# Kernel optimization log

Measured on AMD Instinct MI355X. Metric: run time of the kernel, lower is better.

The kernel has to match this reference:

```python
import jax, jax.numpy as jnp
import numpy as np

B, S, DM, H, SD = 8, 2048, 512, 8, 64
INNER = H * SD
HID = 4 * DM
EPS = 1e-5


def setup_inputs() -> dict:
    key = jax.random.key(0)
    ks = jax.random.split(key, 12)
    p = lambda k, sh: jax.random.normal(k, sh, dtype=jnp.float32) * 0.02
    return {
        "x": jax.random.normal(ks[0], (B, S, DM), dtype=jnp.float32),
        "norm_g": jnp.ones((DM,), jnp.float32),
        "norm_b": jnp.zeros((DM,), jnp.float32),
        "ffn_norm_g": jnp.ones((DM,), jnp.float32),
        "ffn_norm_b": jnp.zeros((DM,), jnp.float32),
        "Wa": p(ks[1], (INNER, DM)),
        "Wb": p(ks[2], (INNER, DM)),
        "Wql": p(ks[3], (INNER, DM)),
        "Wqr": p(ks[4], (INNER, DM)),
        "Wsd": p(ks[5], (H, DM)),
        "bsd": jnp.zeros((H,), jnp.float32),
        "Wpd": p(ks[6], (H, DM)),
        "bpd": jnp.zeros((H,), jnp.float32),
        "Wout": p(ks[7], (DM, INNER)),
        "W1": p(ks[8], (HID, DM)),
        "b1": jnp.zeros((HID,), jnp.float32),
        "W2": p(ks[9], (DM, HID)),
        "b2": jnp.zeros((DM,), jnp.float32),
    }


def _ln(x, g, b):
    m = x.mean(-1, keepdims=True)
    v = ((x - m) ** 2).mean(-1, keepdims=True)
    return (x - m) / jnp.sqrt(v + EPS) * g + b


def reference(x, norm_g, norm_b, ffn_norm_g, ffn_norm_b, Wa, Wb, Wql, Wqr,
              Wsd, bsd, Wpd, bpd, Wout, W1, b1, W2, b2):
    n = _ln(x, norm_g, norm_b)  # [B,S,DM]
    # project, reshape to heads, move time axis first for scan: [S,B,H,SD]
    tm = lambda t: t.reshape(B, S, H, SD).transpose(1, 0, 2, 3)
    a_all = tm(jnp.tanh(n @ Wa.T))
    b_all = tm(jnp.tanh(n @ Wb.T))
    ql_all = tm(jnp.tanh(n @ Wql.T))
    qr_all = tm(jnp.tanh(n @ Wqr.T))
    sd_all = jax.nn.sigmoid(n @ Wsd.T + bsd).transpose(1, 0, 2)[..., None]        # [S,B,H,1]
    pd_all = jax.nn.sigmoid(n @ Wpd.T + bpd).transpose(1, 0, 2)[..., None, None]  # [S,B,H,1,1]

    def step(carry, inp):
        state, pair = carry  # state [B,H,SD], pair [B,H,SD,SD]
        at, bt, qlt, sdt, pdt = inp
        prev = state
        state = sdt * state + (1.0 - sdt) * at
        pair = pdt * pair + (1.0 - pdt) * jnp.einsum('bhd,bhe->bhde', prev, bt)
        lc = jnp.einsum('bhde,bhd->bhe', pair, qlt)  # left context [B,H,SD]
        return (state, pair), lc

    init = (jnp.zeros((B, H, SD), x.dtype), jnp.zeros((B, H, SD, SD), x.dtype))
    _, lc = jax.lax.scan(step, init, (a_all, b_all, ql_all, sd_all, pd_all))  # [S,B,H,SD]

    mixed = ((lc * qr_all).transpose(1, 0, 2, 3).reshape(B, S, INNER)) @ Wout.T  # [B,S,DM]
    r = x + mixed  # dropout is identity in eval
    h = jax.nn.gelu(_ln(r, ffn_norm_g, ffn_norm_b) @ W1.T + b1, approximate=False)
    return r + h @ W2.T + b2
```

## Files before the change

### kernel.cpp

```cpp
#include <hip/hip_runtime.h>
#include <cstdint>
#include <cstddef>

#define B_    8
#define S_    2048
#define DM_   512
#define H_    8
#define SD_   64
#define HID_  2048
#define ROWS  (B_*S_)
#define BH    (B_*H_)
#define NCHUNK 32
#define CLEN   64
#define EPS_  1e-5f

typedef __bf16 bf16x8 __attribute__((ext_vector_type(8)));
typedef float  floatx4 __attribute__((ext_vector_type(4)));

static __device__ __forceinline__ float bf2f(unsigned short h){
  union { unsigned int u; float f; } v; v.u = ((unsigned int)h) << 16; return v.f;
}
static __device__ __forceinline__ unsigned short f2bf(float f){
  union { float f; unsigned int u; } v; v.f = f;
  unsigned int r = v.u + 0x7fffu + ((v.u >> 16) & 1u);
  return (unsigned short)(r >> 16);
}
static __device__ __forceinline__ float fast_tanh(float x){
  float ax = fabsf(x);
  float e  = __expf(2.f*ax);
  float t  = 1.f - 2.f/(e+1.f);
  return copysignf(t, x);
}
static __device__ __forceinline__ float sigmoidf_(float z){
  return 1.f/(1.f + expf(-z));
}
static __device__ __forceinline__ float gelu_exact(float x){
  return 0.5f*x*(1.f + erff(x*0.70710678118654752440f));
}
static __device__ __forceinline__ void gld_lds16(const unsigned short* g, unsigned short* lds){
  __builtin_amdgcn_global_load_lds(
      (const __attribute__((address_space(1))) void*)g,
      (__attribute__((address_space(3))) void*)lds,
      16, 0, 0);
}
static __device__ __forceinline__ int swz(int row, int col){
  return row*64 + (((col>>3) ^ (row&7))<<3) + (col&7);
}

__global__ __launch_bounds__(256) void cvt_weights(
    const float* __restrict__ wa, const float* __restrict__ wb,
    const float* __restrict__ wql, const float* __restrict__ wqr,
    const float* __restrict__ wout, const float* __restrict__ w1,
    const float* __restrict__ w2,
    unsigned short* __restrict__ wcat, unsigned short* __restrict__ woutb,
    unsigned short* __restrict__ w1b, unsigned short* __restrict__ w2b){
  int i = blockIdx.x*256 + threadIdx.x;
  const float* s; unsigned short* d; int base;
  if      (i <  65536){ s=wa;   d=wcat;          base=i; }
  else if (i < 131072){ s=wb;   d=wcat+262144;   base=i-65536; }
  else if (i < 196608){ s=wql;  d=wcat+524288;   base=i-131072; }
  else if (i < 262144){ s=wqr;  d=wcat+786432;   base=i-196608; }
  else if (i < 327680){ s=wout; d=woutb;         base=i-262144; }
  else if (i < 589824){ s=w1;   d=w1b;           base=i-327680; }
  else                { s=w2;   d=w2b;           base=i-589824; }
  float4 v = ((const float4*)s)[base];
  ushort4 o; o.x=f2bf(v.x); o.y=f2bf(v.y); o.z=f2bf(v.z); o.w=f2bf(v.w);
  ((ushort4*)d)[base] = o;
}

__global__ __launch_bounds__(64) void ln_gates(
    const float* __restrict__ x, const float* __restrict__ gam, const float* __restrict__ bet,
    const float* __restrict__ Wsd, const float* __restrict__ bsd,
    const float* __restrict__ Wpd, const float* __restrict__ bpd,
    unsigned short* __restrict__ nbf, float* __restrict__ sdo, float* __restrict__ pdo){
  const int row = blockIdx.x, l = threadIdx.x;
  const float* xr = x + (size_t)row*DM_;
  float4 v0 = ((const float4*)xr)[l*2];
  float4 v1 = ((const float4*)xr)[l*2+1];
  float v[8] = {v0.x,v0.y,v0.z,v0.w,v1.x,v1.y,v1.z,v1.w};
  float s = 0.f;
  #pragma unroll
  for (int i=0;i<8;++i) s += v[i];
  #pragma unroll
  for (int m=1;m<64;m<<=1) s += __shfl_xor(s, m);
  const float mean = s * (1.f/512.f);
  float q = 0.f;
  #pragma unroll
  for (int i=0;i<8;++i){ float d = v[i]-mean; q += d*d; }
  #pragma unroll
  for (int m=1;m<64;m<<=1) q += __shfl_xor(q, m);
  const float rstd = rsqrtf(q*(1.f/512.f) + EPS_);
  float4 g0 = ((const float4*)gam)[l*2], g1 = ((const float4*)gam)[l*2+1];
  float4 b0 = ((const float4*)bet)[l*2], b1 = ((const float4*)bet)[l*2+1];
  float gg[8] = {g0.x,g0.y,g0.z,g0.w,g1.x,g1.y,g1.z,g1.w};
  float bb[8] = {b0.x,b0.y,b0.z,b0.w,b1.x,b1.y,b1.z,b1.w};
  float n[8];
  #pragma unroll
  for (int i=0;i<8;++i) n[i] = (v[i]-mean)*rstd*gg[i] + bb[i];
  ushort4 o0, o1;
  o0.x=f2bf(n[0]); o0.y=f2bf(n[1]); o0.z=f2bf(n[2]); o0.w=f2bf(n[3]);
  o1.x=f2bf(n[4]); o1.y=f2bf(n[5]); o1.z=f2bf(n[6]); o1.w=f2bf(n[7]);
  ((ushort4*)(nbf + (size_t)row*DM_))[l*2]   = o0;
  ((ushort4*)(nbf + (size_t)row*DM_))[l*2+1] = o1;
  float acc[16];
  #pragma unroll
  for (int hh=0; hh<8; ++hh){
    const float4* ws = (const float4*)(Wsd + hh*DM_) + l*2;
    const float4* wp = (const float4*)(Wpd + hh*DM_) + l*2;
    float4 a0=ws[0], a1=ws[1], p0=wp[0], p1=wp[1];
    acc[hh]   = n[0]*a0.x+n[1]*a0.y+n[2]*a0.z+n[3]*a0.w+n[4]*a1.x+n[5]*a1.y+n[6]*a1.z+n[7]*a1.w;
    acc[8+hh] = n[0]*p0.x+n[1]*p0.y+n[2]*p0.z+n[3]*p0.w+n[4]*p1.x+n[5]*p1.y+n[6]*p1.z+n[7]*p1.w;
  }
  #pragma unroll
  for (int k=0;k<16;++k){
    float a = acc[k];
    #pragma unroll
    for (int m=1;m<64;m<<=1) a += __shfl_xor(a, m);
    acc[k] = a;
  }
  if (l==0){
    #pragma unroll
    for (int hh=0; hh<8; ++hh){
      sdo[row*8+hh] = sigmoidf_(acc[hh]   + bsd[hh]);
      pdo[row*8+hh] = sigmoidf_(acc[8+hh] + bpd[hh]);
    }
  }
}

__global__ __launch_bounds__(64) void ln_plain(
    const float* __restrict__ x, const float* __restrict__ gam, const float* __restrict__ bet,
    unsigned short* __restrict__ ob){
  const int row = blockIdx.x, l = threadIdx.x;
  const float* xr = x + (size_t)row*DM_;
  float4 v0 = ((const float4*)xr)[l*2];
  float4 v1 = ((const float4*)xr)[l*2+1];
  float v[8] = {v0.x,v0.y,v0.z,v0.w,v1.x,v1.y,v1.z,v1.w};
  float s = 0.f;
  #pragma unroll
  for (int i=0;i<8;++i) s += v[i];
  #pragma unroll
  for (int m=1;m<64;m<<=1) s += __shfl_xor(s, m);
  const float mean = s * (1.f/512.f);
  float q = 0.f;
  #pragma unroll
  for (int i=0;i<8;++i){ float d = v[i]-mean; q += d*d; }
  #pragma unroll
  for (int m=1;m<64;m<<=1) q += __shfl_xor(q, m);
  const float rstd = rsqrtf(q*(1.f/512.f) + EPS_);
  float4 g0 = ((const float4*)gam)[l*2], g1 = ((const float4*)gam)[l*2+1];
  float4 b0 = ((const float4*)bet)[l*2], b1 = ((const float4*)bet)[l*2+1];
  float gg[8] = {g0.x,g0.y,g0.z,g0.w,g1.x,g1.y,g1.z,g1.w};
  float bb[8] = {b0.x,b0.y,b0.z,b0.w,b1.x,b1.y,b1.z,b1.w};
  ushort4 o0, o1;
  float n0=(v[0]-mean)*rstd*gg[0]+bb[0], n1=(v[1]-mean)*rstd*gg[1]+bb[1];
  float n2=(v[2]-mean)*rstd*gg[2]+bb[2], n3=(v[3]-mean)*rstd*gg[3]+bb[3];
  float n4=(v[4]-mean)*rstd*gg[4]+bb[4], n5=(v[5]-mean)*rstd*gg[5]+bb[5];
  float n6=(v[6]-mean)*rstd*gg[6]+bb[6], n7=(v[7]-mean)*rstd*gg[7]+bb[7];
  o0.x=f2bf(n0); o0.y=f2bf(n1); o0.z=f2bf(n2); o0.w=f2bf(n3);
  o1.x=f2bf(n4); o1.y=f2bf(n5); o1.z=f2bf(n6); o1.w=f2bf(n7);
  ((ushort4*)(ob + (size_t)row*DM_))[l*2]   = o0;
  ((ushort4*)(ob + (size_t)row*DM_))[l*2+1] = o1;
}

template<int MODE>
__global__ __launch_bounds__(256) void gemm128(
    const unsigned short* __restrict__ A, const unsigned short* __restrict__ W,
    const float* __restrict__ bias, const float* __restrict__ resid,
    float* __restrict__ outf, unsigned short* __restrict__ outb,
    int N, int K){
  __shared__ __align__(16) unsigned short As[128*64];
  __shared__ __align__(16) unsigned short Ws[128*64];
  const int tid  = threadIdx.x;
  const int w    = tid >> 6;
  const int lane = tid & 63;
  const int mblk = blockIdx.x, nblk = blockIdx.y;
  const int mrow = (w >> 1) * 64;
  const int ncol = (w & 1) * 64;
  const int fr = lane & 15, fq = lane >> 4;

  int srow[4], scol[4];
  #pragma unroll
  for (int q=0;q<4;++q){
    const int p = q*256 + w*64 + lane;
    srow[q] = p >> 3;
    scol[q] = ((p & 7) ^ (srow[q] & 7)) * 8;
  }

  floatx4 acc[4][4];
  #pragma unroll
  for (int i=0;i<4;++i)
    #pragma unroll
    for (int j=0;j<4;++j)
      acc[i][j] = (floatx4){0.f,0.f,0.f,0.f};

  for (int k0=0; k0<K; k0+=64){
    #pragma unroll
    for (int q=0;q<4;++q){
      gld_lds16(A + (size_t)(mblk*128 + srow[q])*K + k0 + scol[q], As + (q*256 + w*64)*8);
      gld_lds16(W + (size_t)(nblk*128 + srow[q])*K + k0 + scol[q], Ws + (q*256 + w*64)*8);
    }
    __syncthreads();
    #pragma unroll
    for (int kh=0;kh<2;++kh){
      bf16x8 af[4], bf[4];
      #pragma unroll
      for (int i=0;i<4;++i) af[i] = *(const bf16x8*)&As[swz(mrow + i*16 + fr, kh*32 + fq*8)];
      #pragma unroll
      for (int j=0;j<4;++j) bf[j] = *(const bf16x8*)&Ws[swz(ncol + j*16 + fr, kh*32 + fq*8)];
      #pragma unroll
      for (int i=0;i<4;++i)
        #pragma unroll
        for (int j=0;j<4;++j)
          acc[i][j] = __builtin_amdgcn_mfma_f32_16x16x32_bf16(af[i], bf[j], acc[i][j], 0, 0, 0);
    }
    __syncthreads();
  }

  #pragma unroll
  for (int i=0;i<4;++i){
    const int grow_base = mblk*128 + mrow + i*16 + fq*4;
    #pragma unroll
    for (int j=0;j<4;++j){
      const int gcol = nblk*128 + ncol + j*16 + fr;
      float bias_v = 0.f;
      if (MODE==2 || MODE==3) bias_v = bias[gcol];
      #pragma unroll
      for (int r=0;r<4;++r){
        const size_t o = (size_t)(grow_base + r)*N + gcol;
        float v = acc[i][j][r];
        if      (MODE==0) outb[o] = f2bf(fast_tanh(v));
        else if (MODE==1) outf[o] = resid[o] + v;
        else if (MODE==2) outb[o] = f2bf(gelu_exact(v + bias_v));
        else              outf[o] = resid[o] + v + bias_v;
      }
    }
  }
}

__global__ __launch_bounds__(64) void state_local(
    const unsigned short* __restrict__ proj, const float* __restrict__ sdo,
    unsigned short* __restrict__ slocb, float* __restrict__ Sarr,
    float* __restrict__ sEnd){
  const int c = blockIdx.x, bh = blockIdx.y, b = bh>>3, h = bh&7, d = threadIdx.x;
  float s = 0.f, S = 1.f;
  const int t0 = c*CLEN;
  #pragma unroll 4
  for (int j=0;j<CLEN;++j){
    const int t = t0 + j;
    float a  = bf2f(proj[((size_t)(b*S_+t))*2048 + h*64 + d]);
    float sv = sdo[(b*S_+t)*8 + h];
    s = sv*s + (1.f-sv)*a;
    S *= sv;
    slocb[((size_t)bh*S_ + t)*64 + d] = f2bf(s);
    if (d==0) Sarr[bh*S_ + t] = S;
  }
  sEnd[((size_t)c*BH + bh)*64 + d] = s;
}

__global__ __launch_bounds__(64) void state_combine(
    const float* __restrict__ sEnd, const float* __restrict__ Sarr,
    float* __restrict__ sinit){
  const int bh = blockIdx.x, d = threadIdx.x;
  float acc = 0.f;
  for (int c=0;c<NCHUNK;++c){
    sinit[((size_t)c*BH + bh)*64 + d] = acc;
    const int te = c*CLEN + CLEN - 1;
    acc = Sarr[bh*S_ + te]*acc + sEnd[((size_t)c*BH + bh)*64 + d];
  }
}

__global__ __launch_bounds__(256) void prev_mat(
    const unsigned short* __restrict__ slocb, const float* __restrict__ Sarr,
    const float* __restrict__ sinit, unsigned short* __restrict__ prevb){
  const size_t idx = (size_t)blockIdx.x*256 + threadIdx.x;
  const int d  = (int)(idx & 63);
  const size_t bt = idx >> 6;
  const int t  = (int)(bt & (S_-1));
  const int bh = (int)(bt >> 11);
  const int c = t >> 6, j = t & 63;
  float init = sinit[((size_t)c*BH + bh)*64 + d];
  float p;
  if (j==0) p = init;
  else {
    const size_t pt = (size_t)bh*S_ + (t-1);
    p = Sarr[pt]*init + bf2f(slocb[pt*64 + d]);
  }
  prevb[idx] = f2bf(p);
}

__global__ __launch_bounds__(64) void pair_localm(
    const unsigned short* __restrict__ proj, const float* __restrict__ pdo,
    const unsigned short* __restrict__ prevb, float* __restrict__ pairbuf,
    float* __restrict__ Dprod){
  __shared__ __align__(16) unsigned short Bt[4096];
  __shared__ __align__(16) unsigned short Pt[4096];
  const int c=blockIdx.x, bh=blockIdx.y, b=bh>>3, h=bh&7, l=threadIdx.x;
  const int t = c*CLEN + l;
  float pd = pdo[(b*S_+t)*8 + h];
  float D = pd;
  #pragma unroll
  for (int m=1;m<64;m<<=1){ float o = __shfl_up(D, m); if (l>=m) D *= o; }
  const float Dend = __shfl(D, 63);
  const float cu = (Dend / D) * (1.f - pd);
  if (l==63) Dprod[c*BH+bh] = Dend;
  {
    const unsigned short* brow = proj  + ((size_t)(b*S_+t))*2048 + 512 + h*64;
    const unsigned short* prow = prevb + ((size_t)bh*S_ + t)*64;
    #pragma unroll
    for (int e8=0;e8<8;++e8){
      ushort4 u0 = *(const ushort4*)(brow + e8*8);
      ushort4 u1 = *(const ushort4*)(brow + e8*8 + 4);
      unsigned short vs[8] = {u0.x,u0.y,u0.z,u0.w,u1.x,u1.y,u1.z,u1.w};
      ushort4 p0 = *(const ushort4*)(prow + e8*8);
      ushort4 p1 = *(const ushort4*)(prow + e8*8 + 4);
      unsigned short ps[8] = {p0.x,p0.y,p0.z,p0.w,p1.x,p1.y,p1.z,p1.w};
      #pragma unroll
      for (int q=0;q<8;++q){
        const int r = e8*8+q;
        Bt[swz(r, l)] = f2bf(cu * bf2f(vs[q]));
        Pt[swz(r, l)] = ps[q];
      }
    }
  }
  __syncthreads();
  const int fr = l & 15, fq = l >> 4;
  floatx4 acc[4][4];
  #pragma unroll
  for (int i=0;i<4;++i)
    #pragma unroll
    for (int j=0;j<4;++j) acc[i][j] = (floatx4){0.f,0.f,0.f,0.f};
  #pragma unroll
  for (int kh=0;kh<2;++kh){
    bf16x8 af[4], bfr[4];
    #pragma unroll
    for (int i=0;i<4;++i) af[i]  = *(const bf16x8*)&Bt[swz(i*16+fr, kh*32+fq*8)];
    #pragma unroll
    for (int j=0;j<4;++j) bfr[j] = *(const bf16x8*)&Pt[swz(j*16+fr, kh*32+fq*8)];
    #pragma unroll
    for (int i=0;i<4;++i)
      #pragma unroll
      for (int j=0;j<4;++j)
        acc[i][j] = __builtin_amdgcn_mfma_f32_16x16x32_bf16(af[i], bfr[j], acc[i][j], 0, 0, 0);
  }
  float* outp = pairbuf + ((size_t)c*BH + bh)*4096;
  #pragma unroll
  for (int i=0;i<4;++i)
    #pragma unroll
    for (int j=0;j<4;++j)
      #pragma unroll
      for (int r=0;r<4;++r)
        outp[(i*16+fq*4+r)*64 + j*16+fr] = acc[i][j][r];
}

__global__ __launch_bounds__(256) void pair_combine(
    float* __restrict__ pairbuf, const float* __restrict__ Dprod){
  const int idx = blockIdx.x*256 + threadIdx.x;
  const int de = idx & 4095, bh = idx >> 12;
  float acc = 0.f;
  for (int c=0;c<NCHUNK;++c){
    const size_t o = ((size_t)c*BH + bh)*4096 + de;
    float loc = pairbuf[o];
    pairbuf[o] = acc;
    acc = Dprod[c*BH + bh]*acc + loc;
  }
}

__global__ __launch_bounds__(64) void pair_finalm(
    const unsigned short* __restrict__ proj, const float* __restrict__ pdo,
    const unsigned short* __restrict__ prevb, const float* __restrict__ pinit,
    unsigned short* __restrict__ lcqr){
  __shared__ __align__(16) unsigned short Bt[4096];
  __shared__ __align__(16) unsigned short Tb[4096];
  __shared__ __align__(16) float Dtl[64];
  __shared__ __align__(16) float cudl[64];
  const int c=blockIdx.x, bh=blockIdx.y, b=bh>>3, h=bh&7, l=threadIdx.x;
  const int t0 = c*CLEN;
  const int trow = t0 + l;
  float pd = pdo[(b*S_+trow)*8 + h];
  float D = pd;
  #pragma unroll
  for (int m=1;m<64;m<<=1){ float o = __shfl_up(D, m); if (l>=m) D *= o; }
  Dtl[l]  = D;
  cudl[l] = (1.f - pd) / D;
  {
    const unsigned short* brow = proj + ((size_t)(b*S_+trow))*2048 + 512 + h*64;
    #pragma unroll
    for (int e8=0;e8<8;++e8){
      ushort4 u0 = *(const ushort4*)(brow + e8*8);
      ushort4 u1 = *(const ushort4*)(brow + e8*8 + 4);
      unsigned short vs[8] = {u0.x,u0.y,u0.z,u0.w,u1.x,u1.y,u1.z,u1.w};
      #pragma unroll
      for (int q=0;q<8;++q) Bt[swz(e8*8+q, l)] = vs[q];
    }
  }
  __syncthreads();
  const int fr = l & 15, fq = l >> 4;
  bf16x8 qf[4][2], pf[4][2];
  #pragma unroll
  for (int i=0;i<4;++i)
    #pragma unroll
    for (int kh=0;kh<2;++kh){
      qf[i][kh] = *(const bf16x8*)(proj  + ((size_t)(b*S_ + t0 + i*16 + fr))*2048 + 1024 + h*64 + kh*32 + fq*8);
      pf[i][kh] = *(const bf16x8*)(prevb + ((size_t)(bh*S_ + t0 + i*16 + fr))*64  + kh*32 + fq*8);
    }
  floatx4 sacc[4][4];
  #pragma unroll
  for (int i=0;i<4;++i)
    #pragma unroll
    for (int j=0;j<4;++j) sacc[i][j] = (floatx4){0.f,0.f,0.f,0.f};
  #pragma unroll
  for (int kh=0;kh<2;++kh)
    #pragma unroll
    for (int i=0;i<4;++i)
      #pragma unroll
      for (int j=0;j<4;++j)
        sacc[i][j] = __builtin_amdgcn_mfma_f32_16x16x32_bf16(qf[i][kh], pf[j][kh], sacc[i][j], 0, 0, 0);
  float mycud[4];
  #pragma unroll
  for (int j=0;j<4;++j) mycud[j] = cudl[j*16+fr];
  #pragma unroll
  for (int i=0;i<4;++i){
    floatx4 dtv = *(const floatx4*)&Dtl[i*16+fq*4];
    #pragma unroll
    for (int j=0;j<4;++j){
      const int uu = j*16+fr;
      #pragma unroll
      for (int r=0;r<4;++r){
        const int tt = i*16+fq*4+r;
        float v = (uu<=tt) ? (sacc[i][j][r]*dtv[r])*mycud[j] : 0.f;
        Tb[swz(tt, uu)] = f2bf(v);
      }
    }
  }
  __syncthreads();
  floatx4 acc[4][4];
  #pragma unroll
  for (int i=0;i<4;++i)
    #pragma unroll
    for (int j=0;j<4;++j) acc[i][j] = (floatx4){0.f,0.f,0.f,0.f};
  #pragma unroll
  for (int kh=0;kh<2;++kh){
    bf16x8 af[4], bfr[4];
    #pragma unroll
    for (int i=0;i<4;++i) af[i]  = *(const bf16x8*)&Tb[swz(i*16+fr, kh*32+fq*8)];
    #pragma unroll
    for (int j=0;j<4;++j) bfr[j] = *(const bf16x8*)&Bt[swz(j*16+fr, kh*32+fq*8)];
    #pragma unroll
    for (int i=0;i<4;++i)
      #pragma unroll
      for (int j=0;j<4;++j)
        acc[i][j] = __builtin_amdgcn_mfma_f32_16x16x32_bf16(af[i], bfr[j], acc[i][j], 0, 0, 0);
  }
  {
    const float* ibase = pinit + ((size_t)c*BH + bh)*4096;
    #pragma unroll
    for (int kh=0;kh<2;++kh){
      bf16x8 qs[4], inf[4];
      #pragma unroll
      for (int i=0;i<4;++i){
        const float sc = Dtl[i*16+fr];
        #pragma unroll
        for (int e=0;e<8;++e) qs[i][e] = (__bf16)(sc * (float)qf[i][kh][e]);
      }
      #pragma unroll
      for (int j=0;j<4;++j){
        const float* ip = ibase + (j*16+fr)*64 + kh*32 + fq*8;
        float4 f0 = *(const float4*)ip;
        float4 f1 = *(const float4*)(ip+4);
        inf[j][0]=(__bf16)f0.x; inf[j][1]=(__bf16)f0.y; inf[j][2]=(__bf16)f0.z; inf[j][3]=(__bf16)f0.w;
        inf[j][4]=(__bf16)f1.x; inf[j][5]=(__bf16)f1.y; inf[j][6]=(__bf16)f1.z; inf[j][7]=(__bf16)f1.w;
      }
      #pragma unroll
      for (int i=0;i<4;++i)
        #pragma unroll
        for (int j=0;j<4;++j)
          acc[i][j] = __builtin_amdgcn_mfma_f32_16x16x32_bf16(qs[i], inf[j], acc[i][j], 0, 0, 0);
    }
  }
  __syncthreads();
  #pragma unroll
  for (int i=0;i<4;++i)
    #pragma unroll
    for (int j=0;j<4;++j)
      #pragma unroll
      for (int r=0;r<4;++r)
        Tb[swz(i*16+fq*4+r, j*16+fr)] = f2bf(acc[i][j][r]);
  __syncthreads();
  {
    const unsigned short* qrow = proj + ((size_t)(b*S_+trow))*2048 + 1536 + h*64;
    unsigned short* orow = lcqr + ((size_t)(b*S_+trow))*512 + h*64;
    #pragma unroll
    for (int e8=0;e8<8;++e8){
      bf16x8 lcv = *(const bf16x8*)&Tb[swz(l, e8*8)];
      ushort4 q0 = *(const ushort4*)(qrow + e8*8);
      ushort4 q1 = *(const ushort4*)(qrow + e8*8 + 4);
      unsigned short qv[8] = {q0.x,q0.y,q0.z,q0.w,q1.x,q1.y,q1.z,q1.w};
      ushort4 o0, o1;
      o0.x = f2bf((float)lcv[0]*bf2f(qv[0]));
      o0.y = f2bf((float)lcv[1]*bf2f(qv[1]));
      o0.z = f2bf((float)lcv[2]*bf2f(qv[2]));
      o0.w = f2bf((float)lcv[3]*bf2f(qv[3]));
      o1.x = f2bf((float)lcv[4]*bf2f(qv[4]));
      o1.y = f2bf((float)lcv[5]*bf2f(qv[5]));
      o1.z = f2bf((float)lcv[6]*bf2f(qv[6]));
      o1.w = f2bf((float)lcv[7]*bf2f(qv[7]));
      *(ushort4*)(orow + e8*8)     = o0;
      *(ushort4*)(orow + e8*8 + 4) = o1;
    }
  }
}

extern "C" void kernel_launch(void* const* d_in, const int* in_sizes, int n_in,
                              void* d_out, int out_size, void* d_ws, size_t ws_size,
                              hipStream_t stream){
  (void)in_sizes; (void)n_in; (void)out_size; (void)ws_size;
  const float* x    = (const float*)d_in[0];
  const float* ng   = (const float*)d_in[1];
  const float* nb   = (const float*)d_in[2];
  const float* fng  = (const float*)d_in[3];
  const float* fnb  = (const float*)d_in[4];
  const float* Wa   = (const float*)d_in[5];
  const float* Wb   = (const float*)d_in[6];
  const float* Wql  = (const float*)d_in[7];
  const float* Wqr  = (const float*)d_in[8];
  const float* Wsd  = (const float*)d_in[9];
  const float* bsd  = (const float*)d_in[10];
  const float* Wpd  = (const float*)d_in[11];
  const float* bpd  = (const float*)d_in[12];
  const float* Wout = (const float*)d_in[13];
  const float* W1   = (const float*)d_in[14];
  const float* b1   = (const float*)d_in[15];
  const float* W2   = (const float*)d_in[16];
  const float* b2   = (const float*)d_in[17];
  float* out = (float*)d_out;
  char* ws = (char*)d_ws;

  size_t off = 0;
  auto alloc = [&](size_t bytes)->char*{ char* p = ws + off; off += (bytes + 255) & ~(size_t)255; return p; };
  char* RA = alloc((size_t)ROWS*DM_*2);
  char* RB = alloc((size_t)ROWS*2048*2);
  char* RD = alloc((size_t)BH*S_*64*4);
  char* RE = alloc((size_t)BH*S_*64*4);
  float* sdo   = (float*)alloc((size_t)ROWS*8*4);
  float* pdo   = (float*)alloc((size_t)ROWS*8*4);
  float* Sarr  = (float*)alloc((size_t)BH*S_*4);
  float* sinit = (float*)alloc((size_t)NCHUNK*BH*64*4);
  float* sEnd  = (float*)alloc((size_t)NCHUNK*BH*64*4);
  float* dprod = (float*)alloc((size_t)NCHUNK*BH*4);
  unsigned short* wcat  = (unsigned short*)alloc((size_t)2048*512*2);
  unsigned short* woutb = (unsigned short*)alloc((size_t)512*512*2);
  unsigned short* w1b   = (unsigned short*)alloc((size_t)2048*512*2);
  unsigned short* w2b   = (unsigned short*)alloc((size_t)512*2048*2);

  unsigned short* nbf   = (unsigned short*)RA;
  unsigned short* lcqr  = (unsigned short*)RA;
  unsigned short* nr    = (unsigned short*)RA;
  unsigned short* proj  = (unsigned short*)RB;
  unsigned short* hbuf  = (unsigned short*)RB;
  unsigned short* slocb = (unsigned short*)RD;
  float* pairb = (float*)RD;
  unsigned short* prevb = (unsigned short*)RE;
  float* rbuf  = (float*)RE;

  cvt_weights<<<dim3(3328), dim3(256), 0, stream>>>(Wa,Wb,Wql,Wqr,Wout,W1,W2, wcat,woutb,w1b,w2b);
  ln_gates<<<dim3(ROWS), dim3(64), 0, stream>>>(x, ng, nb, Wsd, bsd, Wpd, bpd, nbf, sdo, pdo);
  gemm128<0><<<dim3(128,16), dim3(256), 0, stream>>>(nbf, wcat, nullptr, nullptr, nullptr, proj, 2048, 512);
  state_local<<<dim3(NCHUNK,BH), dim3(64), 0, stream>>>(proj, sdo, slocb, Sarr, sEnd);
  state_combine<<<dim3(BH), dim3(64), 0, stream>>>(sEnd, Sarr, sinit);
  prev_mat<<<dim3(32768), dim3(256), 0, stream>>>(slocb, Sarr, sinit, prevb);
  pair_localm<<<dim3(NCHUNK,BH), dim3(64), 0, stream>>>(proj, pdo, prevb, pairb, dprod);
  pair_combine<<<dim3(1024), dim3(256), 0, stream>>>(pairb, dprod);
  pair_finalm<<<dim3(NCHUNK,BH), dim3(64), 0, stream>>>(proj, pdo, prevb, pairb, lcqr);
  gemm128<1><<<dim3(128,4), dim3(256), 0, stream>>>(lcqr, woutb, nullptr, x, rbuf, nullptr, 512, 512);
  ln_plain<<<dim3(ROWS), dim3(64), 0, stream>>>(rbuf, fng, fnb, nr);
  gemm128<2><<<dim3(128,16), dim3(256), 0, stream>>>(nr, w1b, b1, nullptr, nullptr, hbuf, 2048, 512);
  gemm128<3><<<dim3(128,4), dim3(256), 0, stream>>>(hbuf, w2b, b2, rbuf, out, nullptr, 512, 2048);
}
```

Baseline: 446.2 us.

## Use 256x256 tiles for wide GEMMs and store residual in bf16

Adds a gemm256 kernel with 512-thread blocks and 256x256 output tiles, used for the two N=2048 projections (QKV-like tanh projection and FFN up with GELU). Each block loads twice as many rows and columns per K step, so operand reuse per LDS load goes up and global traffic goes down. Separately, the residual buffer r is now stored as bf16 instead of fp32, which halves its write and read traffic in the Wout GEMM, the LayerNorm and the final GEMM. The cost is more registers per thread and fewer blocks (512 per GEMM), plus bf16 rounding of the residual stream added to the output.

```diff
diff --git a/kernel.cpp b/kernel.cpp
--- a/kernel.cpp
+++ b/kernel.cpp
@@ -128,13 +128,14 @@
 }
 
 __global__ __launch_bounds__(64) void ln_plain(
-    const float* __restrict__ x, const float* __restrict__ gam, const float* __restrict__ bet,
+    const unsigned short* __restrict__ xb, const float* __restrict__ gam, const float* __restrict__ bet,
     unsigned short* __restrict__ ob){
   const int row = blockIdx.x, l = threadIdx.x;
-  const float* xr = x + (size_t)row*DM_;
-  float4 v0 = ((const float4*)xr)[l*2];
-  float4 v1 = ((const float4*)xr)[l*2+1];
-  float v[8] = {v0.x,v0.y,v0.z,v0.w,v1.x,v1.y,v1.z,v1.w};
+  const unsigned short* xr = xb + (size_t)row*DM_ + l*8;
+  ushort4 u0 = *(const ushort4*)xr;
+  ushort4 u1 = *(const ushort4*)(xr+4);
+  float v[8] = {bf2f(u0.x),bf2f(u0.y),bf2f(u0.z),bf2f(u0.w),
+                bf2f(u1.x),bf2f(u1.y),bf2f(u1.z),bf2f(u1.w)};
   float s = 0.f;
   #pragma unroll
   for (int i=0;i<8;++i) s += v[i];
@@ -152,20 +153,91 @@
   float gg[8] = {g0.x,g0.y,g0.z,g0.w,g1.x,g1.y,g1.z,g1.w};
   float bb[8] = {b0.x,b0.y,b0.z,b0.w,b1.x,b1.y,b1.z,b1.w};
   ushort4 o0, o1;
-  float n0=(v[0]-mean)*rstd*gg[0]+bb[0], n1=(v[1]-mean)*rstd*gg[1]+bb[1];
-  float n2=(v[2]-mean)*rstd*gg[2]+bb[2], n3=(v[3]-mean)*rstd*gg[3]+bb[3];
-  float n4=(v[4]-mean)*rstd*gg[4]+bb[4], n5=(v[5]-mean)*rstd*gg[5]+bb[5];
-  float n6=(v[6]-mean)*rstd*gg[6]+bb[6], n7=(v[7]-mean)*rstd*gg[7]+bb[7];
-  o0.x=f2bf(n0); o0.y=f2bf(n1); o0.z=f2bf(n2); o0.w=f2bf(n3);
-  o1.x=f2bf(n4); o1.y=f2bf(n5); o1.z=f2bf(n6); o1.w=f2bf(n7);
+  o0.x=f2bf((v[0]-mean)*rstd*gg[0]+bb[0]); o0.y=f2bf((v[1]-mean)*rstd*gg[1]+bb[1]);
+  o0.z=f2bf((v[2]-mean)*rstd*gg[2]+bb[2]); o0.w=f2bf((v[3]-mean)*rstd*gg[3]+bb[3]);
+  o1.x=f2bf((v[4]-mean)*rstd*gg[4]+bb[4]); o1.y=f2bf((v[5]-mean)*rstd*gg[5]+bb[5]);
+  o1.z=f2bf((v[6]-mean)*rstd*gg[6]+bb[6]); o1.w=f2bf((v[7]-mean)*rstd*gg[7]+bb[7]);
   ((ushort4*)(ob + (size_t)row*DM_))[l*2]   = o0;
   ((ushort4*)(ob + (size_t)row*DM_))[l*2+1] = o1;
+}
+
+template<int MODE>
+__global__ __launch_bounds__(512, 2) void gemm256(
+    const unsigned short* __restrict__ A, const unsigned short* __restrict__ W,
+    const float* __restrict__ bias, unsigned short* __restrict__ outb,
+    int N, int K){
+  __shared__ __align__(16) unsigned short As[256*64];
+  __shared__ __align__(16) unsigned short Ws[256*64];
+  const int tid  = threadIdx.x;
+  const int w    = tid >> 6;
+  const int lane = tid & 63;
+  const int mblk = blockIdx.x, nblk = blockIdx.y;
+  const int mrow = (w >> 1) * 64;
+  const int ncol = (w & 1) * 128;
+  const int fr = lane & 15, fq = lane >> 4;
+
+  int srow[4], scol[4];
+  #pragma unroll
+  for (int q=0;q<4;++q){
+    const int p = q*512 + tid;
+    srow[q] = p >> 3;
+    scol[q] = ((p & 7) ^ (srow[q] & 7)) * 8;
+  }
+
+  floatx4 acc[4][8];
+  #pragma unroll
+  for (int i=0;i<4;++i)
+    #pragma unroll
+    for (int j=0;j<8;++j)
+      acc[i][j] = (floatx4){0.f,0.f,0.f,0.f};
+
+  for (int k0=0; k0<K; k0+=64){
+    #pragma unroll
+    for (int q=0;q<4;++q){
+      gld_lds16(A + (size_t)(mblk*256 + srow[q])*K + k0 + scol[q], As + (q*512 + tid)*8);
+      gld_lds16(W + (size_t)(nblk*256 + srow[q])*K + k0 + scol[q], Ws + (q*512 + tid)*8);
+    }
+    __syncthreads();
+    #pragma unroll
+    for (int kh=0;kh<2;++kh){
+      bf16x8 af[4], bf[8];
+      #pragma unroll
+      for (int i=0;i<4;++i) af[i] = *(const bf16x8*)&As[swz(mrow + i*16 + fr, kh*32 + fq*8)];
+      #pragma unroll
+      for (int j=0;j<8;++j) bf[j] = *(const bf16x8*)&Ws[swz(ncol + j*16 + fr, kh*32 + fq*8)];
+      #pragma unroll
+      for (int i=0;i<4;++i)
+        #pragma unroll
+        for (int j=0;j<8;++j)
+          acc[i][j] = __builtin_amdgcn_mfma_f32_16x16x32_bf16(af[i], bf[j], acc[i][j], 0, 0, 0);
+    }
+    __syncthreads();
+  }
+
+  #pragma unroll
+  for (int i=0;i<4;++i){
+    const int grow_base = mblk*256 + mrow + i*16 + fq*4;
+    #pragma unroll
+    for (int j=0;j<8;++j){
+      const int gcol = nblk*256 + ncol + j*16 + fr;
+      float bias_v = 0.f;
+      if (MODE==2) bias_v = bias[gcol];
+      #pragma unroll
+      for (int r=0;r<4;++r){
+        const size_t o = (size_t)(grow_base + r)*N + gcol;
+        float v = acc[i][j][r];
+        if (MODE==0) outb[o] = f2bf(fast_tanh(v));
+        else         outb[o] = f2bf(gelu_exact(v + bias_v));
+      }
+    }
+  }
 }
 
 template<int MODE>
 __global__ __launch_bounds__(256) void gemm128(
     const unsigned short* __restrict__ A, const unsigned short* __restrict__ W,
-    const float* __restrict__ bias, const float* __restrict__ resid,
+    const float* __restrict__ bias, const float* __restrict__ residf,
+    const unsigned short* __restrict__ residb,
     float* __restrict__ outf, unsigned short* __restrict__ outb,
     int N, int K){
   __shared__ __align__(16) unsigned short As[128*64];
@@ -223,15 +295,13 @@
     for (int j=0;j<4;++j){
       const int gcol = nblk*128 + ncol + j*16 + fr;
       float bias_v = 0.f;
-      if (MODE==2 || MODE==3) bias_v = bias[gcol];
+      if (MODE==3) bias_v = bias[gcol];
       #pragma unroll
       for (int r=0;r<4;++r){
         const size_t o = (size_t)(grow_base + r)*N + gcol;
         float v = acc[i][j][r];
-        if      (MODE==0) outb[o] = f2bf(fast_tanh(v));
-        else if (MODE==1) outf[o] = resid[o] + v;
-        else if (MODE==2) outb[o] = f2bf(gelu_exact(v + bias_v));
-        else              outf[o] = resid[o] + v + bias_v;
+        if (MODE==1) outb[o] = f2bf(residf[o] + v);
+        else         outf[o] = bf2f(residb[o]) + v + bias_v;
       }
     }
   }
@@ -560,19 +630,19 @@
   unsigned short* slocb = (unsigned short*)RD;
   float* pairb = (float*)RD;
   unsigned short* prevb = (unsigned short*)RE;
-  float* rbuf  = (float*)RE;
+  unsigned short* rbufb = (unsigned short*)RE;
 
   cvt_weights<<<dim3(3328), dim3(256), 0, stream>>>(Wa,Wb,Wql,Wqr,Wout,W1,W2, wcat,woutb,w1b,w2b);
   ln_gates<<<dim3(ROWS), dim3(64), 0, stream>>>(x, ng, nb, Wsd, bsd, Wpd, bpd, nbf, sdo, pdo);
-  gemm128<0><<<dim3(128,16), dim3(256), 0, stream>>>(nbf, wcat, nullptr, nullptr, nullptr, proj, 2048, 512);
+  gemm256<0><<<dim3(64,8), dim3(512), 0, stream>>>(nbf, wcat, nullptr, proj, 2048, 512);
   state_local<<<dim3(NCHUNK,BH), dim3(64), 0, stream>>>(proj, sdo, slocb, Sarr, sEnd);
   state_combine<<<dim3(BH), dim3(64), 0, stream>>>(sEnd, Sarr, sinit);
   prev_mat<<<dim3(32768), dim3(256), 0, stream>>>(slocb, Sarr, sinit, prevb);
   pair_localm<<<dim3(NCHUNK,BH), dim3(64), 0, stream>>>(proj, pdo, prevb, pairb, dprod);
   pair_combine<<<dim3(1024), dim3(256), 0, stream>>>(pairb, dprod);
   pair_finalm<<<dim3(NCHUNK,BH), dim3(64), 0, stream>>>(proj, pdo, prevb, pairb, lcqr);
-  gemm128<1><<<dim3(128,4), dim3(256), 0, stream>>>(lcqr, woutb, nullptr, x, rbuf, nullptr, 512, 512);
-  ln_plain<<<dim3(ROWS), dim3(64), 0, stream>>>(rbuf, fng, fnb, nr);
-  gemm128<2><<<dim3(128,16), dim3(256), 0, stream>>>(nr, w1b, b1, nullptr, nullptr, hbuf, 2048, 512);
-  gemm128<3><<<dim3(128,4), dim3(256), 0, stream>>>(hbuf, w2b, b2, rbuf, out, nullptr, 512, 2048);
-}
+  gemm128<1><<<dim3(128,4), dim3(256), 0, stream>>>(lcqr, woutb, nullptr, x, nullptr, nullptr, rbufb, 512, 512);
+  ln_plain<<<dim3(ROWS), dim3(64), 0, stream>>>(rbufb, fng, fnb, nr);
+  gemm256<2><<<dim3(64,8), dim3(512), 0, stream>>>(nr, w1b, b1, hbuf, 2048, 512);
+  gemm128<3><<<dim3(128,4), dim3(256), 0, stream>>>(hbuf, w2b, b2, nullptr, rbufb, out, nullptr, 512, 2048);
+}
```

Result: no change. 449.3 us (+0.7%).

## Double-buffer GEMM shared-memory tiles and store residual stream in bf16

Applied to the files above, without the earlier changes.

The GEMM kernel now keeps two LDS buffers and issues the global-to-LDS loads for the next K tile before computing the current one, so each iteration needs one barrier instead of two and load latency can overlap the MFMA work. Separately, the post-attention residual buffer is stored as bf16 instead of fp32, which halves its write traffic and the reads in the FFN layernorm and final GEMM epilogue. The residual change costs precision in the skip connection that feeds the output, and the double buffer doubles LDS use per block, which may lower occupancy.

```diff
diff --git a/kernel.cpp b/kernel.cpp
--- a/kernel.cpp
+++ b/kernel.cpp
@@ -128,13 +128,14 @@
 }
 
 __global__ __launch_bounds__(64) void ln_plain(
-    const float* __restrict__ x, const float* __restrict__ gam, const float* __restrict__ bet,
+    const unsigned short* __restrict__ xb, const float* __restrict__ gam, const float* __restrict__ bet,
     unsigned short* __restrict__ ob){
   const int row = blockIdx.x, l = threadIdx.x;
-  const float* xr = x + (size_t)row*DM_;
-  float4 v0 = ((const float4*)xr)[l*2];
-  float4 v1 = ((const float4*)xr)[l*2+1];
-  float v[8] = {v0.x,v0.y,v0.z,v0.w,v1.x,v1.y,v1.z,v1.w};
+  const unsigned short* xr = xb + (size_t)row*DM_ + l*8;
+  ushort4 u0 = *(const ushort4*)xr;
+  ushort4 u1 = *(const ushort4*)(xr+4);
+  float v[8] = {bf2f(u0.x),bf2f(u0.y),bf2f(u0.z),bf2f(u0.w),
+                bf2f(u1.x),bf2f(u1.y),bf2f(u1.z),bf2f(u1.w)};
   float s = 0.f;
   #pragma unroll
   for (int i=0;i<8;++i) s += v[i];
@@ -152,24 +153,23 @@
   float gg[8] = {g0.x,g0.y,g0.z,g0.w,g1.x,g1.y,g1.z,g1.w};
   float bb[8] = {b0.x,b0.y,b0.z,b0.w,b1.x,b1.y,b1.z,b1.w};
   ushort4 o0, o1;
-  float n0=(v[0]-mean)*rstd*gg[0]+bb[0], n1=(v[1]-mean)*rstd*gg[1]+bb[1];
-  float n2=(v[2]-mean)*rstd*gg[2]+bb[2], n3=(v[3]-mean)*rstd*gg[3]+bb[3];
-  float n4=(v[4]-mean)*rstd*gg[4]+bb[4], n5=(v[5]-mean)*rstd*gg[5]+bb[5];
-  float n6=(v[6]-mean)*rstd*gg[6]+bb[6], n7=(v[7]-mean)*rstd*gg[7]+bb[7];
-  o0.x=f2bf(n0); o0.y=f2bf(n1); o0.z=f2bf(n2); o0.w=f2bf(n3);
-  o1.x=f2bf(n4); o1.y=f2bf(n5); o1.z=f2bf(n6); o1.w=f2bf(n7);
+  o0.x=f2bf((v[0]-mean)*rstd*gg[0]+bb[0]); o0.y=f2bf((v[1]-mean)*rstd*gg[1]+bb[1]);
+  o0.z=f2bf((v[2]-mean)*rstd*gg[2]+bb[2]); o0.w=f2bf((v[3]-mean)*rstd*gg[3]+bb[3]);
+  o1.x=f2bf((v[4]-mean)*rstd*gg[4]+bb[4]); o1.y=f2bf((v[5]-mean)*rstd*gg[5]+bb[5]);
+  o1.z=f2bf((v[6]-mean)*rstd*gg[6]+bb[6]); o1.w=f2bf((v[7]-mean)*rstd*gg[7]+bb[7]);
   ((ushort4*)(ob + (size_t)row*DM_))[l*2]   = o0;
   ((ushort4*)(ob + (size_t)row*DM_))[l*2+1] = o1;
 }
 
 template<int MODE>
-__global__ __launch_bounds__(256) void gemm128(
+__global__ __launch_bounds__(256) void gemm128db(
     const unsigned short* __restrict__ A, const unsigned short* __restrict__ W,
-    const float* __restrict__ bias, const float* __restrict__ resid,
+    const float* __restrict__ bias, const float* __restrict__ residf,
+    const unsigned short* __restrict__ residb,
     float* __restrict__ outf, unsigned short* __restrict__ outb,
     int N, int K){
-  __shared__ __align__(16) unsigned short As[128*64];
-  __shared__ __align__(16) unsigned short Ws[128*64];
+  __shared__ __align__(16) unsigned short As[2][128*64];
+  __shared__ __align__(16) unsigned short Ws[2][128*64];
   const int tid  = threadIdx.x;
   const int w    = tid >> 6;
   const int lane = tid & 63;
@@ -193,27 +193,37 @@
     for (int j=0;j<4;++j)
       acc[i][j] = (floatx4){0.f,0.f,0.f,0.f};
 
-  for (int k0=0; k0<K; k0+=64){
-    #pragma unroll
-    for (int q=0;q<4;++q){
-      gld_lds16(A + (size_t)(mblk*128 + srow[q])*K + k0 + scol[q], As + (q*256 + w*64)*8);
-      gld_lds16(W + (size_t)(nblk*128 + srow[q])*K + k0 + scol[q], Ws + (q*256 + w*64)*8);
-    }
+  #pragma unroll
+  for (int q=0;q<4;++q){
+    gld_lds16(A + (size_t)(mblk*128 + srow[q])*K + scol[q], As[0] + (q*256 + w*64)*8);
+    gld_lds16(W + (size_t)(nblk*128 + srow[q])*K + scol[q], Ws[0] + (q*256 + w*64)*8);
+  }
+
+  const int nk = K >> 6;
+  for (int it=0; it<nk; ++it){
+    const int cur = it & 1;
     __syncthreads();
+    if (it+1 < nk){
+      const int k1 = (it+1) << 6;
+      #pragma unroll
+      for (int q=0;q<4;++q){
+        gld_lds16(A + (size_t)(mblk*128 + srow[q])*K + k1 + scol[q], As[1-cur] + (q*256 + w*64)*8);
+        gld_lds16(W + (size_t)(nblk*128 + srow[q])*K + k1 + scol[q], Ws[1-cur] + (q*256 + w*64)*8);
+      }
+    }
     #pragma unroll
     for (int kh=0;kh<2;++kh){
       bf16x8 af[4], bf[4];
       #pragma unroll
-      for (int i=0;i<4;++i) af[i] = *(const bf16x8*)&As[swz(mrow + i*16 + fr, kh*32 + fq*8)];
-      #pragma unroll
-      for (int j=0;j<4;++j) bf[j] = *(const bf16x8*)&Ws[swz(ncol + j*16 + fr, kh*32 + fq*8)];
+      for (int i=0;i<4;++i) af[i] = *(const bf16x8*)&As[cur][swz(mrow + i*16 + fr, kh*32 + fq*8)];
+      #pragma unroll
+      for (int j=0;j<4;++j) bf[j] = *(const bf16x8*)&Ws[cur][swz(ncol + j*16 + fr, kh*32 + fq*8)];
       #pragma unroll
       for (int i=0;i<4;++i)
         #pragma unroll
         for (int j=0;j<4;++j)
           acc[i][j] = __builtin_amdgcn_mfma_f32_16x16x32_bf16(af[i], bf[j], acc[i][j], 0, 0, 0);
     }
-    __syncthreads();
   }
 
   #pragma unroll
@@ -229,9 +239,9 @@
         const size_t o = (size_t)(grow_base + r)*N + gcol;
         float v = acc[i][j][r];
         if      (MODE==0) outb[o] = f2bf(fast_tanh(v));
-        else if (MODE==1) outf[o] = resid[o] + v;
+        else if (MODE==1) outb[o] = f2bf(residf[o] + v);
         else if (MODE==2) outb[o] = f2bf(gelu_exact(v + bias_v));
-        else              outf[o] = resid[o] + v + bias_v;
+        else              outf[o] = bf2f(residb[o]) + v + bias_v;
       }
     }
   }
@@ -560,19 +570,19 @@
   unsigned short* slocb = (unsigned short*)RD;
   float* pairb = (float*)RD;
   unsigned short* prevb = (unsigned short*)RE;
-  float* rbuf  = (float*)RE;
+  unsigned short* rbufb = (unsigned short*)RE;
 
   cvt_weights<<<dim3(3328), dim3(256), 0, stream>>>(Wa,Wb,Wql,Wqr,Wout,W1,W2, wcat,woutb,w1b,w2b);
   ln_gates<<<dim3(ROWS), dim3(64), 0, stream>>>(x, ng, nb, Wsd, bsd, Wpd, bpd, nbf, sdo, pdo);
-  gemm128<0><<<dim3(128,16), dim3(256), 0, stream>>>(nbf, wcat, nullptr, nullptr, nullptr, proj, 2048, 512);
+  gemm128db<0><<<dim3(128,16), dim3(256), 0, stream>>>(nbf, wcat, nullptr, nullptr, nullptr, nullptr, proj, 2048, 512);
   state_local<<<dim3(NCHUNK,BH), dim3(64), 0, stream>>>(proj, sdo, slocb, Sarr, sEnd);
   state_combine<<<dim3(BH), dim3(64), 0, stream>>>(sEnd, Sarr, sinit);
   prev_mat<<<dim3(32768), dim3(256), 0, stream>>>(slocb, Sarr, sinit, prevb);
   pair_localm<<<dim3(NCHUNK,BH), dim3(64), 0, stream>>>(proj, pdo, prevb, pairb, dprod);
   pair_combine<<<dim3(1024), dim3(256), 0, stream>>>(pairb, dprod);
   pair_finalm<<<dim3(NCHUNK,BH), dim3(64), 0, stream>>>(proj, pdo, prevb, pairb, lcqr);
-  gemm128<1><<<dim3(128,4), dim3(256), 0, stream>>>(lcqr, woutb, nullptr, x, rbuf, nullptr, 512, 512);
-  ln_plain<<<dim3(ROWS), dim3(64), 0, stream>>>(rbuf, fng, fnb, nr);
-  gemm128<2><<<dim3(128,16), dim3(256), 0, stream>>>(nr, w1b, b1, nullptr, nullptr, hbuf, 2048, 512);
-  gemm128<3><<<dim3(128,4), dim3(256), 0, stream>>>(hbuf, w2b, b2, rbuf, out, nullptr, 512, 2048);
-}
+  gemm128db<1><<<dim3(128,4), dim3(256), 0, stream>>>(lcqr, woutb, nullptr, x, nullptr, nullptr, rbufb, 512, 512);
+  ln_plain<<<dim3(ROWS), dim3(64), 0, stream>>>(rbufb, fng, fnb, nr);
+  gemm128db<2><<<dim3(128,16), dim3(256), 0, stream>>>(nr, w1b, b1, nullptr, nullptr, nullptr, hbuf, 2048, 512);
+  gemm128db<3><<<dim3(128,4), dim3(256), 0, stream>>>(hbuf, w2b, b2, nullptr, rbufb, out, nullptr, 512, 2048);
+}
```

Result: faster. 436.8 us (-2.1%).
